# Optimization experiments

Measured on AMD Instinct MI355X. Metric: run time of the kernel, lower is better.

## Reference

```python
import jax, jax.numpy as jnp
import numpy as np

B, S, D, H = 2, 2048, 1024, 16
HD = D // H  # 64

def setup_inputs() -> dict:
    key = jax.random.key(0)
    k1, k2, k3 = jax.random.split(key, 3)
    hidden_states = jax.random.normal(k1, (B, S, D), dtype=jnp.float32)
    w_attn = jax.random.normal(k2, (D, 3 * D), dtype=jnp.float32) * 0.02
    w_proj = jax.random.normal(k3, (D, D), dtype=jnp.float32) * 0.02
    return {"hidden_states": hidden_states, "w_attn": w_attn, "w_proj": w_proj}

def reference(hidden_states, w_attn, w_proj):
    b, s, d = hidden_states.shape
    # c_attn: Conv1D (bias is a scalar zero in the source)
    qkv = jnp.einsum('bsd,de->bse', hidden_states, w_attn)  # [B,S,3D]
    q, k, v = jnp.split(qkv, 3, axis=-1)
    def split_heads(t):
        return t.reshape(b, s, H, HD).transpose(0, 2, 1, 3)  # [B,H,S,HD]
    q, k, v = split_heads(q), split_heads(k), split_heads(v)
    # eager attention; scale_attn_weights=True -> divide by sqrt(head_dim)
    scores = jnp.einsum('bhqd,bhkd->bhqk', q, k) / jnp.sqrt(jnp.float32(HD))
    # NOTE: source registers bias buffer as all-ones (True), so the causal
    # torch.where is a no-op -- faithfully no masking is applied.
    probs = jax.nn.softmax(scores, axis=-1)
    attn = jnp.einsum('bhqk,bhkd->bhqd', probs, v)  # [B,H,S,HD]
    attn = attn.transpose(0, 2, 1, 3).reshape(b, s, d)  # merge heads
    out = jnp.einsum('bsd,de->bse', attn, w_proj)  # c_proj (zero bias)
    return out
```

## Files before the change

### kernel.cpp

```cpp
#include <hip/hip_runtime.h>
#include <hip/hip_bf16.h>

typedef __attribute__((ext_vector_type(8))) short bf16x8;
typedef __attribute__((ext_vector_type(4))) short short4v;
typedef __attribute__((ext_vector_type(4))) float f32x4;
typedef __attribute__((ext_vector_type(16))) float f32x16;
typedef __attribute__((ext_vector_type(4))) float float4v;

__device__ __forceinline__ short f2bf(float f) {
    union { float f; unsigned u; } v; v.f = f;
    unsigned r = v.u + 0x7fffu + ((v.u >> 16) & 1u);
    return (short)(r >> 16);
}
__device__ __forceinline__ float bf2f(short s) {
    union { unsigned u; float f; } v;
    v.u = ((unsigned)(unsigned short)s) << 16;
    return v.f;
}

__device__ __forceinline__ void gload16(const short* g, short* lds) {
    __builtin_amdgcn_global_load_lds(
        (const __attribute__((address_space(1))) unsigned*)g,
        (__attribute__((address_space(3))) unsigned*)lds, 16, 0, 0);
}

__global__ __launch_bounds__(256) void cvt_bf16x8(const float* __restrict__ in,
                                                  short* __restrict__ out) {
    int i = (blockIdx.x * 256 + threadIdx.x) * 8;
    float4v a0 = *reinterpret_cast<const float4v*>(&in[i]);
    float4v a1 = *reinterpret_cast<const float4v*>(&in[i + 4]);
    bf16x8 s;
    s[0] = f2bf(a0[0]); s[1] = f2bf(a0[1]); s[2] = f2bf(a0[2]); s[3] = f2bf(a0[3]);
    s[4] = f2bf(a1[0]); s[5] = f2bf(a1[1]); s[6] = f2bf(a1[2]); s[7] = f2bf(a1[3]);
    *reinterpret_cast<bf16x8*>(&out[i]) = s;
}

__global__ __launch_bounds__(256) void tconv(const float* __restrict__ in,
                                             short* __restrict__ out,
                                             int Kdim, int Ndim) {
    __shared__ int Ls[64][65];
    const int t = threadIdx.x;
    const int k0 = blockIdx.y * 64, n0 = blockIdx.x * 64;
    const int kl = t >> 4, n4 = (t & 15) * 4;
#pragma unroll
    for (int it = 0; it < 4; ++it) {
        int k = kl + it * 16;
        float4v v = *reinterpret_cast<const float4v*>(&in[(size_t)(k0 + k) * Ndim + n0 + n4]);
#pragma unroll
        for (int c = 0; c < 4; ++c) Ls[k][n4 + c] = (int)(unsigned short)f2bf(v[c]);
    }
    __syncthreads();
    const int nl0 = t >> 4, kq = (t & 15) * 4;
#pragma unroll
    for (int it = 0; it < 4; ++it) {
        int nl = nl0 + it * 16;
        short4v s;
#pragma unroll
        for (int j = 0; j < 4; ++j) s[j] = (short)Ls[kq + j][nl];
        *reinterpret_cast<short4v*>(&out[(size_t)(n0 + nl) * Kdim + k0 + kq]) = s;
    }
}

__global__ __launch_bounds__(256) void qkv_gemm(const short* __restrict__ Ah,
                                                const short* __restrict__ Wt,
                                                short* __restrict__ Qw,
                                                short* __restrict__ Kw,
                                                short* __restrict__ Vt) {
    __shared__ short As[128 * 64];
    __shared__ short Bs[128 * 64];
    const int tid = threadIdx.x;
    const int l = tid & 63, w = tid >> 6;
    const int g = l >> 4, lr = l & 15;
    const int r8 = l >> 3, sl = l & 7;
    const int xs = (sl ^ r8) * 8;
    const int wm = (w >> 1) * 64, wn = (w & 1) * 64;
    const int bid = blockIdx.x;
    const int xcd = bid & 7, idx = bid >> 3;
    const int nt = (xcd & 1) * 12 + idx % 12;
    const int mt = (xcd >> 1) * 8 + idx / 12;
    const int m0 = mt * 128;
    const int n0 = nt * 128;
    const bool isV = (n0 >= 2048);
    f32x4 acc[4][4] = {};
    for (int k0 = 0; k0 < 1024; k0 += 64) {
        const short* Ag = Ah + m0 * 1024 + k0;
        const short* Bg = Wt + n0 * 1024 + k0;
#pragma unroll
        for (int i = 0; i < 4; ++i) {
            int seg = w * 4 + i;
            gload16(Ag + (seg * 8 + r8) * 1024 + xs, &As[seg * 512]);
            gload16(Bg + (seg * 8 + r8) * 1024 + xs, &Bs[seg * 512]);
        }
        __syncthreads();
#pragma unroll
        for (int kk = 0; kk < 2; ++kk) {
            bf16x8 af[4], bfr[4];
#pragma unroll
            for (int mi = 0; mi < 4; ++mi) {
                int row = wm + mi * 16 + lr;
                af[mi] = *reinterpret_cast<const bf16x8*>(&As[row * 64 + (((4 * kk + g) ^ (lr & 7)) * 8)]);
            }
#pragma unroll
            for (int ni = 0; ni < 4; ++ni) {
                int col = wn + ni * 16 + lr;
                bfr[ni] = *reinterpret_cast<const bf16x8*>(&Bs[col * 64 + (((4 * kk + g) ^ (lr & 7)) * 8)]);
            }
            if (isV) {
#pragma unroll
                for (int mi = 0; mi < 4; ++mi)
#pragma unroll
                    for (int ni = 0; ni < 4; ++ni)
                        acc[mi][ni] = __builtin_amdgcn_mfma_f32_16x16x32_bf16(af[mi], bfr[ni], acc[mi][ni], 0, 0, 0);
            } else {
#pragma unroll
                for (int mi = 0; mi < 4; ++mi)
#pragma unroll
                    for (int ni = 0; ni < 4; ++ni)
                        acc[mi][ni] = __builtin_amdgcn_mfma_f32_16x16x32_bf16(bfr[ni], af[mi], acc[mi][ni], 0, 0, 0);
            }
        }
        __syncthreads();
    }
    if (isV) {
#pragma unroll
        for (int mi = 0; mi < 4; ++mi) {
            int m = m0 + wm + mi * 16 + g * 4;
            int bb = m >> 11, s0 = m & 2047;
#pragma unroll
            for (int ni = 0; ni < 4; ++ni) {
                int n = n0 + wn + ni * 16 + lr;
                int hh = (n >> 6) & 15, d = n & 63;
                short4v pv;
#pragma unroll
                for (int r = 0; r < 4; ++r) pv[r] = f2bf(acc[mi][ni][r]);
                *reinterpret_cast<short4v*>(&Vt[(((bb * 16 + hh) * 64) + d) * 2048 + s0]) = pv;
            }
        }
    } else {
        const bool isQ = (n0 < 1024);
        const float sc = isQ ? 0.18033688011112042f : 1.0f;
        short* dst = isQ ? Qw : Kw;
#pragma unroll
        for (int mi = 0; mi < 4; ++mi) {
            int m = m0 + wm + mi * 16 + lr;
            int bb = m >> 11, s0 = m & 2047;
#pragma unroll
            for (int ni = 0; ni < 4; ++ni) {
                int n = n0 + wn + ni * 16 + g * 4;
                int hh = (n >> 6) & 15, d = n & 63;
                float a0 = acc[mi][ni][0] * sc, a1 = acc[mi][ni][1] * sc;
                float a2 = acc[mi][ni][2] * sc, a3 = acc[mi][ni][3] * sc;
                int w0, w1;
                asm("v_cvt_pk_bf16_f32 %0, %1, %2" : "=v"(w0) : "v"(a0), "v"(a1));
                asm("v_cvt_pk_bf16_f32 %0, %1, %2" : "=v"(w1) : "v"(a2), "v"(a3));
                union { int wd[2]; short4v s; } u;
                u.wd[0] = w0; u.wd[1] = w1;
                *reinterpret_cast<short4v*>(&dst[((bb * 16 + hh) * 2048 + s0) * 64 + d]) = u.s;
            }
        }
    }
}

__global__ __launch_bounds__(256, 4) void attn6s(const short* __restrict__ Qw,
                                                 const short* __restrict__ Kw,
                                                 const short* __restrict__ Vt,
                                                 short* __restrict__ N0,
                                                 short* __restrict__ N1,
                                                 float* __restrict__ Tot) {
    __shared__ short Ks[2][64 * 64];
    __shared__ short Vs[2][64 * 64];
    const int tid = threadIdx.x;
    const int w = tid >> 6, l = tid & 63;
    const int q = l & 31, hi = l >> 5;
    const int r8 = l >> 3, sl = l & 7;
    const int xs = (sl ^ r8) * 8;
    const int bid = blockIdx.x;
    const int work = (bid & 7) * 128 + (bid >> 3);
    const int head = work >> 5;
    const int qblk = (work & 31) >> 1;
    const int ks = work & 1;
    const int b = head >> 4, h = head & 15;
    const int q0 = qblk * 128 + w * 32;
    const short* Qb = Qw + ((b * 16 + h) * 2048 + q0) * 64;
    const short* Kb = Kw + ((b * 16 + h) * 2048 + ks * 1024) * 64;
    const short* Vb = Vt + ((b * 16 + h) * 64) * 2048 + ks * 1024;

    bf16x8 qb[4];
#pragma unroll
    for (int c = 0; c < 4; ++c)
        qb[c] = *reinterpret_cast<const bf16x8*>(&Qb[q * 64 + c * 16 + hi * 8]);

    f32x16 o0 = {}, o1 = {};
    float psum = 0.f;

#define STAGE_KV(buf, j0)                                                        \
    {                                                                            \
        _Pragma("unroll")                                                        \
        for (int i = 0; i < 2; ++i) {                                            \
            int seg = w * 2 + i;                                                 \
            gload16(Kb + ((j0) + seg * 8 + r8) * 64 + xs, &Ks[buf][seg * 512]);  \
            gload16(Vb + (seg * 8 + r8) * 2048 + (j0) + xs, &Vs[buf][seg * 512]);\
        }                                                                        \
    }

    STAGE_KV(0, 0);
    __syncthreads();
    int cur = 0;

    for (int jt = 0; jt < 16; ++jt) {
        if (jt < 15) STAGE_KV(cur ^ 1, (jt + 1) * 64);

#pragma unroll
        for (int sub = 0; sub < 2; ++sub) {
            f32x16 st = {};
#pragma unroll
            for (int c = 0; c < 4; ++c) {
                bf16x8 ka = *reinterpret_cast<const bf16x8*>(
                    &Ks[cur][(sub * 32 + q) * 64 + (((2 * c + hi) ^ (q & 7)) * 8)]);
                st = __builtin_amdgcn_mfma_f32_32x32x16_bf16(ka, qb[c], st, 0, 0, 0);
            }
            float p[16];
#pragma unroll
            for (int r = 0; r < 16; ++r) p[r] = __builtin_amdgcn_exp2f(st[r]);
            float s01 = (p[0] + p[1]) + (p[2] + p[3]);
            float s23 = (p[4] + p[5]) + (p[6] + p[7]);
            float s45 = (p[8] + p[9]) + (p[10] + p[11]);
            float s67 = (p[12] + p[13]) + (p[14] + p[15]);
            psum += (s01 + s23) + (s45 + s67);
            int pk[4][2];
#pragma unroll
            for (int bq = 0; bq < 4; ++bq) {
                int w0, w1;
                asm("v_cvt_pk_bf16_f32 %0, %1, %2" : "=v"(w0) : "v"(p[4 * bq]), "v"(p[4 * bq + 1]));
                asm("v_cvt_pk_bf16_f32 %0, %1, %2" : "=v"(w1) : "v"(p[4 * bq + 2]), "v"(p[4 * bq + 3]));
                pk[bq][0] = w0; pk[bq][1] = w1;
            }
#pragma unroll
            for (int c2 = 0; c2 < 2; ++c2) {
                int w0 = pk[2 * c2][0], w2 = pk[2 * c2 + 1][0];
                int w1 = pk[2 * c2][1], w3 = pk[2 * c2 + 1][1];
                asm("v_permlane32_swap_b32 %0, %1" : "+v"(w0), "+v"(w2));
                asm("v_permlane32_swap_b32 %0, %1" : "+v"(w1), "+v"(w3));
                union { int wd[4]; bf16x8 v; } pb;
                pb.wd[0] = w0; pb.wd[1] = w1; pb.wd[2] = w2; pb.wd[3] = w3;
#pragma unroll
                for (int dt = 0; dt < 2; ++dt) {
                    bf16x8 va = *reinterpret_cast<const bf16x8*>(
                        &Vs[cur][(dt * 32 + q) * 64 + (((4 * sub + 2 * c2 + hi) ^ (q & 7)) * 8)]);
                    if (dt == 0) o0 = __builtin_amdgcn_mfma_f32_32x32x16_bf16(va, pb.v, o0, 0, 0, 0);
                    else         o1 = __builtin_amdgcn_mfma_f32_32x32x16_bf16(va, pb.v, o1, 0, 0, 0);
                }
            }
        }
        __syncthreads();
        cur ^= 1;
    }
#undef STAGE_KV

    int pa = __float_as_int(psum), pb2 = pa;
    asm("v_permlane32_swap_b32 %0, %1" : "+v"(pa), "+v"(pb2));
    float tot = __int_as_float(pa) + __int_as_float(pb2);
    float inv = 1.f / tot;

    short* Nd = ks ? N1 : N0;
    short* Orow = &Nd[(b * 2048 + q0 + q) * 1024 + h * 64];
#pragma unroll
    for (int r = 0; r < 4; ++r) {
        short4v ov0, ov1;
#pragma unroll
        for (int j = 0; j < 4; ++j) {
            ov0[j] = f2bf(o0[4 * r + j] * inv);
            ov1[j] = f2bf(o1[4 * r + j] * inv);
        }
        *reinterpret_cast<short4v*>(&Orow[8 * r + 4 * hi]) = ov0;
        *reinterpret_cast<short4v*>(&Orow[32 + 8 * r + 4 * hi]) = ov1;
    }
    if (hi == 0)
        Tot[ks * 65536 + (b * 16 + h) * 2048 + q0 + q] = tot;
}

__global__ __launch_bounds__(256) void attn_merge(short* __restrict__ N0,
                                                  const short* __restrict__ N1,
                                                  const float* __restrict__ Tot) {
    int i = (blockIdx.x * 256 + threadIdx.x) * 8;
    int bs = i >> 10;
    int b = bs >> 11, s = bs & 2047;
    int h = (i >> 6) & 15;
    int qi = (b * 16 + h) * 2048 + s;
    float t0 = Tot[qi], t1 = Tot[65536 + qi];
    float inv = 1.f / (t0 + t1);
    float w0 = t0 * inv, w1 = t1 * inv;
    bf16x8 a = *reinterpret_cast<const bf16x8*>(&N0[i]);
    bf16x8 c = *reinterpret_cast<const bf16x8*>(&N1[i]);
    bf16x8 r;
#pragma unroll
    for (int j = 0; j < 8; ++j) r[j] = f2bf(bf2f(a[j]) * w0 + bf2f(c[j]) * w1);
    *reinterpret_cast<bf16x8*>(&N0[i]) = r;
}

__global__ __launch_bounds__(256) void proj_gemm(const short* __restrict__ Ag,
                                                 const short* __restrict__ Wtp,
                                                 float* __restrict__ Out) {
    __shared__ short As[128 * 64];
    __shared__ short Bs[128 * 64];
    const int tid = threadIdx.x;
    const int l = tid & 63, w = tid >> 6;
    const int g = l >> 4, lr = l & 15;
    const int r8 = l >> 3, sl = l & 7;
    const int xs = (sl ^ r8) * 8;
    const int wm = (w >> 1) * 64, wn = (w & 1) * 64;
    const int bid = blockIdx.x;
    const int xcd = bid & 7, idx = bid >> 3;
    const int nt = (xcd & 1) * 4 + (idx & 3);
    const int mt = (xcd >> 1) * 8 + (idx >> 2);
    const int m0 = mt * 128;
    const int n0 = nt * 128;
    f32x4 acc[4][4] = {};
    for (int k0 = 0; k0 < 1024; k0 += 64) {
        const short* Ab = Ag + m0 * 1024 + k0;
        const short* Bg = Wtp + n0 * 1024 + k0;
#pragma unroll
        for (int i = 0; i < 4; ++i) {
            int seg = w * 4 + i;
            gload16(Ab + (seg * 8 + r8) * 1024 + xs, &As[seg * 512]);
            gload16(Bg + (seg * 8 + r8) * 1024 + xs, &Bs[seg * 512]);
        }
        __syncthreads();
#pragma unroll
        for (int kk = 0; kk < 2; ++kk) {
            bf16x8 af[4], bfr[4];
#pragma unroll
            for (int mi = 0; mi < 4; ++mi) {
                int row = wm + mi * 16 + lr;
                af[mi] = *reinterpret_cast<const bf16x8*>(&As[row * 64 + (((4 * kk + g) ^ (lr & 7)) * 8)]);
            }
#pragma unroll
            for (int ni = 0; ni < 4; ++ni) {
                int col = wn + ni * 16 + lr;
                bfr[ni] = *reinterpret_cast<const bf16x8*>(&Bs[col * 64 + (((4 * kk + g) ^ (lr & 7)) * 8)]);
            }
#pragma unroll
            for (int mi = 0; mi < 4; ++mi)
#pragma unroll
                for (int ni = 0; ni < 4; ++ni)
                    acc[mi][ni] = __builtin_amdgcn_mfma_f32_16x16x32_bf16(af[mi], bfr[ni], acc[mi][ni], 0, 0, 0);
        }
        __syncthreads();
    }
#pragma unroll
    for (int mi = 0; mi < 4; ++mi) {
#pragma unroll
        for (int ni = 0; ni < 4; ++ni) {
            int n = n0 + wn + ni * 16 + lr;
#pragma unroll
            for (int r = 0; r < 4; ++r) {
                int mm = m0 + wm + mi * 16 + g * 4 + r;
                Out[mm * 1024 + n] = acc[mi][ni][r];
            }
        }
    }
}

extern "C" void kernel_launch(void* const* d_in, const int* in_sizes, int n_in,
                              void* d_out, int out_size, void* d_ws, size_t ws_size,
                              hipStream_t stream) {
    const float* hidden = (const float*)d_in[0];
    const float* w_attn = (const float*)d_in[1];
    const float* w_proj = (const float*)d_in[2];
    float* out = (float*)d_out;

    short* AhN0 = (short*)d_ws;
    short* Qw = AhN0 + 4194304;
    short* Kw = Qw + 4194304;
    short* Vt = Kw + 4194304;
    short* Wta = (short*)d_out;
    float* Tot = (float*)((char*)d_out + 7u * 1024 * 1024);
    short* N1 = (short*)((char*)d_out + 8u * 1024 * 1024);

    cvt_bf16x8<<<dim3(2048), 256, 0, stream>>>(hidden, AhN0);
    tconv<<<dim3(48, 16), 256, 0, stream>>>(w_attn, Wta, 1024, 3072);
    qkv_gemm<<<dim3(768), 256, 0, stream>>>(AhN0, Wta, Qw, Kw, Vt);
    attn6s<<<dim3(1024), 256, 0, stream>>>(Qw, Kw, Vt, AhN0, N1, Tot);
    attn_merge<<<dim3(2048), 256, 0, stream>>>(AhN0, N1, Tot);
    tconv<<<dim3(16, 16), 256, 0, stream>>>(w_proj, Qw, 1024, 1024);
    proj_gemm<<<dim3(256), 256, 0, stream>>>(AhN0, Qw, out);
}
```

Before: 131.6 us.

## Merge prep and post elementwise kernels and add MFMA priority hints in attention

Fuses the hidden-state bf16 conversion with the w_attn transpose into one launch, and the split-KV merge with the w_proj transpose into another, cutting the kernel count from seven to five. In the attention loop, LDS offsets are precomputed once, and MFMA sections are bracketed with s_setprio to favor matrix issue across waves. The launch fusion removes per-launch gaps and lets independent work overlap. Branching inside a block grid carries little risk, but setprio may reorder waves unpredictably.

Result: faster. 126.1 us (-4.2%).

```diff
diff --git a/kernel.cpp b/kernel.cpp
--- a/kernel.cpp
+++ b/kernel.cpp
@@ -24,23 +24,11 @@
         (__attribute__((address_space(3))) unsigned*)lds, 16, 0, 0);
 }
 
-__global__ __launch_bounds__(256) void cvt_bf16x8(const float* __restrict__ in,
-                                                  short* __restrict__ out) {
-    int i = (blockIdx.x * 256 + threadIdx.x) * 8;
-    float4v a0 = *reinterpret_cast<const float4v*>(&in[i]);
-    float4v a1 = *reinterpret_cast<const float4v*>(&in[i + 4]);
-    bf16x8 s;
-    s[0] = f2bf(a0[0]); s[1] = f2bf(a0[1]); s[2] = f2bf(a0[2]); s[3] = f2bf(a0[3]);
-    s[4] = f2bf(a1[0]); s[5] = f2bf(a1[1]); s[6] = f2bf(a1[2]); s[7] = f2bf(a1[3]);
-    *reinterpret_cast<bf16x8*>(&out[i]) = s;
-}
-
-__global__ __launch_bounds__(256) void tconv(const float* __restrict__ in,
-                                             short* __restrict__ out,
-                                             int Kdim, int Ndim) {
+__device__ __forceinline__ void tconv_tile(const float* __restrict__ in,
+                                           short* __restrict__ out,
+                                           int Kdim, int Ndim, int n0, int k0) {
     __shared__ int Ls[64][65];
     const int t = threadIdx.x;
-    const int k0 = blockIdx.y * 64, n0 = blockIdx.x * 64;
     const int kl = t >> 4, n4 = (t & 15) * 4;
 #pragma unroll
     for (int it = 0; it < 4; ++it) {
@@ -58,6 +46,26 @@
 #pragma unroll
         for (int j = 0; j < 4; ++j) s[j] = (short)Ls[kq + j][nl];
         *reinterpret_cast<short4v*>(&out[(size_t)(n0 + nl) * Kdim + k0 + kq]) = s;
+    }
+}
+
+__global__ __launch_bounds__(256) void prep1(const float* __restrict__ hidden,
+                                             short* __restrict__ Ah,
+                                             const float* __restrict__ w_attn,
+                                             short* __restrict__ Wta) {
+    const int bx = blockIdx.x;
+    if (bx < 2048) {
+        int i = (bx * 256 + threadIdx.x) * 8;
+        float4v a0 = *reinterpret_cast<const float4v*>(&hidden[i]);
+        float4v a1 = *reinterpret_cast<const float4v*>(&hidden[i + 4]);
+        bf16x8 s;
+        s[0] = f2bf(a0[0]); s[1] = f2bf(a0[1]); s[2] = f2bf(a0[2]); s[3] = f2bf(a0[3]);
+        s[4] = f2bf(a1[0]); s[5] = f2bf(a1[1]); s[6] = f2bf(a1[2]); s[7] = f2bf(a1[3]);
+        *reinterpret_cast<bf16x8*>(&Ah[i]) = s;
+    } else {
+        int idx = bx - 2048;
+        int n0 = (idx % 48) * 64, k0 = (idx / 48) * 64;
+        tconv_tile(w_attn, Wta, 1024, 3072, n0, k0);
     }
 }
 
@@ -190,6 +198,20 @@
     for (int c = 0; c < 4; ++c)
         qb[c] = *reinterpret_cast<const bf16x8*>(&Qb[q * 64 + c * 16 + hi * 8]);
 
+    int koff[2][4], voff[2][2][2];
+#pragma unroll
+    for (int sub = 0; sub < 2; ++sub)
+#pragma unroll
+        for (int c = 0; c < 4; ++c)
+            koff[sub][c] = (sub * 32 + q) * 64 + (((2 * c + hi) ^ (q & 7)) * 8);
+#pragma unroll
+    for (int sub = 0; sub < 2; ++sub)
+#pragma unroll
+        for (int c2 = 0; c2 < 2; ++c2)
+#pragma unroll
+            for (int dt = 0; dt < 2; ++dt)
+                voff[sub][c2][dt] = (dt * 32 + q) * 64 + (((4 * sub + 2 * c2 + hi) ^ (q & 7)) * 8);
+
     f32x16 o0 = {}, o1 = {};
     float psum = 0.f;
 
@@ -213,12 +235,13 @@
 #pragma unroll
         for (int sub = 0; sub < 2; ++sub) {
             f32x16 st = {};
+            __builtin_amdgcn_s_setprio(1);
 #pragma unroll
             for (int c = 0; c < 4; ++c) {
-                bf16x8 ka = *reinterpret_cast<const bf16x8*>(
-                    &Ks[cur][(sub * 32 + q) * 64 + (((2 * c + hi) ^ (q & 7)) * 8)]);
+                bf16x8 ka = *reinterpret_cast<const bf16x8*>(&Ks[cur][koff[sub][c]]);
                 st = __builtin_amdgcn_mfma_f32_32x32x16_bf16(ka, qb[c], st, 0, 0, 0);
             }
+            __builtin_amdgcn_s_setprio(0);
             float p[16];
 #pragma unroll
             for (int r = 0; r < 16; ++r) p[r] = __builtin_amdgcn_exp2f(st[r]);
@@ -243,13 +266,14 @@
                 asm("v_permlane32_swap_b32 %0, %1" : "+v"(w1), "+v"(w3));
                 union { int wd[4]; bf16x8 v; } pb;
                 pb.wd[0] = w0; pb.wd[1] = w1; pb.wd[2] = w2; pb.wd[3] = w3;
+                __builtin_amdgcn_s_setprio(1);
 #pragma unroll
                 for (int dt = 0; dt < 2; ++dt) {
-                    bf16x8 va = *reinterpret_cast<const bf16x8*>(
-                        &Vs[cur][(dt * 32 + q) * 64 + (((4 * sub + 2 * c2 + hi) ^ (q & 7)) * 8)]);
+                    bf16x8 va = *reinterpret_cast<const bf16x8*>(&Vs[cur][voff[sub][c2][dt]]);
                     if (dt == 0) o0 = __builtin_amdgcn_mfma_f32_32x32x16_bf16(va, pb.v, o0, 0, 0, 0);
                     else         o1 = __builtin_amdgcn_mfma_f32_32x32x16_bf16(va, pb.v, o1, 0, 0, 0);
                 }
+                __builtin_amdgcn_s_setprio(0);
             }
         }
         __syncthreads();
@@ -279,23 +303,32 @@
         Tot[ks * 65536 + (b * 16 + h) * 2048 + q0 + q] = tot;
 }
 
-__global__ __launch_bounds__(256) void attn_merge(short* __restrict__ N0,
-                                                  const short* __restrict__ N1,
-                                                  const float* __restrict__ Tot) {
-    int i = (blockIdx.x * 256 + threadIdx.x) * 8;
-    int bs = i >> 10;
-    int b = bs >> 11, s = bs & 2047;
-    int h = (i >> 6) & 15;
-    int qi = (b * 16 + h) * 2048 + s;
-    float t0 = Tot[qi], t1 = Tot[65536 + qi];
-    float inv = 1.f / (t0 + t1);
-    float w0 = t0 * inv, w1 = t1 * inv;
-    bf16x8 a = *reinterpret_cast<const bf16x8*>(&N0[i]);
-    bf16x8 c = *reinterpret_cast<const bf16x8*>(&N1[i]);
-    bf16x8 r;
-#pragma unroll
-    for (int j = 0; j < 8; ++j) r[j] = f2bf(bf2f(a[j]) * w0 + bf2f(c[j]) * w1);
-    *reinterpret_cast<bf16x8*>(&N0[i]) = r;
+__global__ __launch_bounds__(256) void post(short* __restrict__ N0,
+                                            const short* __restrict__ N1,
+                                            const float* __restrict__ Tot,
+                                            const float* __restrict__ w_proj,
+                                            short* __restrict__ Wtp) {
+    const int bx = blockIdx.x;
+    if (bx < 2048) {
+        int i = (bx * 256 + threadIdx.x) * 8;
+        int bs = i >> 10;
+        int b = bs >> 11, s = bs & 2047;
+        int h = (i >> 6) & 15;
+        int qi = (b * 16 + h) * 2048 + s;
+        float t0 = Tot[qi], t1 = Tot[65536 + qi];
+        float inv = 1.f / (t0 + t1);
+        float w0 = t0 * inv, w1 = t1 * inv;
+        bf16x8 a = *reinterpret_cast<const bf16x8*>(&N0[i]);
+        bf16x8 c = *reinterpret_cast<const bf16x8*>(&N1[i]);
+        bf16x8 r;
+#pragma unroll
+        for (int j = 0; j < 8; ++j) r[j] = f2bf(bf2f(a[j]) * w0 + bf2f(c[j]) * w1);
+        *reinterpret_cast<bf16x8*>(&N0[i]) = r;
+    } else {
+        int idx = bx - 2048;
+        int n0 = (idx % 16) * 64, k0 = (idx / 16) * 64;
+        tconv_tile(w_proj, Wtp, 1024, 1024, n0, k0);
+    }
 }
 
 __global__ __launch_bounds__(256) void proj_gemm(const short* __restrict__ Ag,
@@ -377,11 +410,9 @@
     float* Tot = (float*)((char*)d_out + 7u * 1024 * 1024);
     short* N1 = (short*)((char*)d_out + 8u * 1024 * 1024);
 
-    cvt_bf16x8<<<dim3(2048), 256, 0, stream>>>(hidden, AhN0);
-    tconv<<<dim3(48, 16), 256, 0, stream>>>(w_attn, Wta, 1024, 3072);
+    prep1<<<dim3(2816), 256, 0, stream>>>(hidden, AhN0, w_attn, Wta);
     qkv_gemm<<<dim3(768), 256, 0, stream>>>(AhN0, Wta, Qw, Kw, Vt);
     attn6s<<<dim3(1024), 256, 0, stream>>>(Qw, Kw, Vt, AhN0, N1, Tot);
-    attn_merge<<<dim3(2048), 256, 0, stream>>>(AhN0, N1, Tot);
-    tconv<<<dim3(16, 16), 256, 0, stream>>>(w_proj, Qw, 1024, 1024);
+    post<<<dim3(2304), 256, 0, stream>>>(AhN0, N1, Tot, w_proj, Qw);
     proj_gemm<<<dim3(256), 256, 0, stream>>>(AhN0, Qw, out);
 }
```
